# Performance work log

Hardware: AMD Instinct MI355X
Metric: run time of the kernel (lower is better)

The kernel has to match this reference:

```python
import jax, jax.numpy as jnp
import numpy as np

B, C, L, CH, CW = 2, 8, 512, 256, 8
NH = 8
FEATURES = 256
ROT = FEATURES // NH  # 32, partial rotary dim


def _rope(x, rot_dim):
    # x: (..., l, hd); rotate first rot_dim dims (interleaved pairs), pass rest through
    l = x.shape[-2]
    inv_freq = 1.0 / (10000.0 ** (jnp.arange(0, rot_dim, 2, dtype=jnp.float32) / rot_dim))
    freqs = jnp.arange(l, dtype=jnp.float32)[:, None] * inv_freq[None, :]  # (l, rot/2)
    freqs = jnp.repeat(freqs, 2, axis=-1)  # (l, rot)
    cos, sin = jnp.cos(freqs), jnp.sin(freqs)
    xr, xp = x[..., :rot_dim], x[..., rot_dim:]
    x2 = xr.reshape(xr.shape[:-1] + (rot_dim // 2, 2))
    rot = jnp.stack((-x2[..., 1], x2[..., 0]), axis=-1).reshape(xr.shape)
    return jnp.concatenate([xr * cos + rot * sin, xp], axis=-1)


def _conv(z, w):
    return jax.lax.conv_general_dilated(z, w, (1, 1), ((1, 1), (1, 1)),
                                        dimension_numbers=('NCHW', 'OIHW', 'NCHW'))


def _mlin(z, w):
    # per-channel linear over the height (features) axis: (n,c,h,w) x (c,g,h) -> (n,c,g,w)
    return jnp.einsum('nchw,cgh->ncgw', z, w)


def setup_inputs() -> dict:
    key = jax.random.key(0)
    ks = jax.random.split(key, 10)
    s_conv = 1.0 / np.sqrt(C * 9)
    s_lin = 1.0 / np.sqrt(FEATURES)
    return {
        'x': jax.random.normal(ks[0], (B, C, L, CH, CW), jnp.float32),
        'prev_qk': jax.random.normal(ks[1], (B, C, NH, L, L), jnp.float32),
        'conv_q_w': jax.random.normal(ks[2], (C, C, 3, 3), jnp.float32) * s_conv,
        'conv_k_w': jax.random.normal(ks[3], (C, C, 3, 3), jnp.float32) * s_conv,
        'conv_v_w': jax.random.normal(ks[4], (C, C, 3, 3), jnp.float32) * s_conv,
        'wq': jax.random.normal(ks[5], (C, FEATURES, FEATURES), jnp.float32) * s_lin,
        'wk': jax.random.normal(ks[6], (C, FEATURES, FEATURES), jnp.float32) * s_lin,
        'wv': jax.random.normal(ks[7], (C, FEATURES, FEATURES), jnp.float32) * s_lin,
        'wo': jax.random.normal(ks[8], (C, FEATURES, FEATURES), jnp.float32) * s_lin,
    }


def reference(x, prev_qk, conv_q_w, conv_k_w, conv_v_w, wq, wk, wv, wo):
    b, c, l, ch, cw = x.shape
    h = x.transpose(0, 2, 1, 3, 4).reshape(b * l, c, ch, cw)

    def heads(z):  # (b*l,c,ch,cw) -> (b,c,NH,l,hd)
        return (z.reshape(b, l, c, ch * cw).transpose(0, 2, 1, 3)
                 .reshape(b, c, l, NH, -1).transpose(0, 1, 3, 2, 4))

    q = heads(_mlin(_conv(h, conv_q_w), wq))
    k = heads(_mlin(_conv(h, conv_k_w), wk))
    v = heads(_mlin(_conv(h, conv_v_w), wv))

    q = _rope(q, ROT)
    k = _rope(k, ROT)

    qk = jnp.einsum('bcnld,bcnmd->bcnlm', q, k) / jnp.sqrt(jnp.float32(ch)) + prev_qk
    a = jnp.einsum('bcnlm,bcnmd->bcnld', jax.nn.softmax(qk, axis=-1), v)
    a = a.transpose(0, 1, 3, 2, 4).reshape(b, c, l, ch, cw)

    out = (_mlin(a.transpose(0, 2, 1, 3, 4).reshape(b * l, c, ch, cw), wo)
           .reshape(b, l, c, ch, cw).transpose(0, 2, 1, 3, 4))
    return out, qk
```

## Files before the change

kernel.cpp:

```cpp
#include <hip/hip_runtime.h>
#include <cstddef>
#include <cstdint>


typedef unsigned short u16;
typedef unsigned int u32;
typedef __attribute__((ext_vector_type(8))) short short8;
typedef __attribute__((ext_vector_type(4))) float floatx4;

__device__ __forceinline__ float bf2f(u16 u) {
  union { u32 i; float f; } v; v.i = ((u32)u) << 16; return v.f;
}
__device__ __forceinline__ u16 f2bf(float f) {
  union { float f; u32 i; } v; v.f = f;
  return (u16)((v.i + 0x7fffu + ((v.i >> 16) & 1u)) >> 16);
}

__global__ __launch_bounds__(256) void convert_w_kernel(
    const float* __restrict__ wq, const float* __restrict__ wk,
    const float* __restrict__ wv, const float* __restrict__ wo,
    u16* __restrict__ wbf) {
  int mat = blockIdx.y;
  const float* src = (mat == 0) ? wq : (mat == 1) ? wk : (mat == 2) ? wv : wo;
  int idx = blockIdx.x * 256 + threadIdx.x;
  wbf[(size_t)mat * 524288 + idx] = f2bf(src[idx]);
}

__global__ __launch_bounds__(256) void conv_fused_kernel(
    const float* __restrict__ x,
    const float* __restrict__ wq, const float* __restrict__ wk,
    const float* __restrict__ wv,
    u16* __restrict__ oq, u16* __restrict__ ok, u16* __restrict__ ov) {
  __shared__ float wl[1728];
  int t = threadIdx.x;
  for (int i2 = t; i2 < 1728; i2 += 256)
    wl[i2] = (i2 < 576) ? wq[i2] : (i2 < 1152 ? wk[i2 - 576] : wv[i2 - 1152]);
  __syncthreads();

  int bl = blockIdx.x >> 1, ih = blockIdx.x & 1;
  int b = bl >> 9, l = bl & 511;
  int il = t & 127, sh = t >> 7;
  int i = ih * 128 + il;

  float acc[12][8];
#pragma unroll
  for (int p = 0; p < 12; ++p)
#pragma unroll
    for (int j = 0; j < 8; ++j) acc[p][j] = 0.f;

  for (int ci = 0; ci < 8; ++ci) {
    const float* xc = x + (((size_t)(b * 8 + ci) * 512 + l) << 11);
    float xr[3][10];
#pragma unroll
    for (int di = 0; di < 3; ++di) {
      int gi = i + di - 1;
      xr[di][0] = 0.f; xr[di][9] = 0.f;
      if (gi >= 0 && gi < 256) {
        float4 a = *(const float4*)(xc + gi * 8);
        float4 bq = *(const float4*)(xc + gi * 8 + 4);
        xr[di][1] = a.x; xr[di][2] = a.y; xr[di][3] = a.z; xr[di][4] = a.w;
        xr[di][5] = bq.x; xr[di][6] = bq.y; xr[di][7] = bq.z; xr[di][8] = bq.w;
      } else {
#pragma unroll
        for (int j = 1; j < 9; ++j) xr[di][j] = 0.f;
      }
    }
#pragma unroll
    for (int p = 0; p < 12; ++p) {
      int pp = sh * 12 + p;
      int s = pp >> 3, co = pp & 7;
      const float* wp = &wl[s * 576 + (co * 8 + ci) * 9];
      float w00 = wp[0], w01 = wp[1], w02 = wp[2];
      float w10 = wp[3], w11 = wp[4], w12 = wp[5];
      float w20 = wp[6], w21 = wp[7], w22 = wp[8];
#pragma unroll
      for (int j = 0; j < 8; ++j) {
        acc[p][j] += w00 * xr[0][j] + w01 * xr[0][j + 1] + w02 * xr[0][j + 2]
                   + w10 * xr[1][j] + w11 * xr[1][j + 1] + w12 * xr[1][j + 2]
                   + w20 * xr[2][j] + w21 * xr[2][j + 1] + w22 * xr[2][j + 2];
      }
    }
  }
#pragma unroll
  for (int p = 0; p < 12; ++p) {
    int pp = sh * 12 + p;
    int s = pp >> 3, co = pp & 7;
    u16* ob = (s == 0) ? oq : (s == 1) ? ok : ov;
    size_t base = ((size_t)(bl * 8 + co)) << 11;
#pragma unroll
    for (int j = 0; j < 8; ++j) ob[base + j * 256 + i] = f2bf(acc[p][j]);
  }
}

template <int MODE>
__global__ __launch_bounds__(256) void mlin_mfma_kernel(
    const u16* __restrict__ zin,
    const u16* __restrict__ wbf,
    void* __restrict__ outp) {
  __shared__ u16 lds_a[8192];
  __shared__ u16 lds_b[8192];

  int tid = threadIdx.x;
  int wv = tid >> 6, lane = tid & 63;
  int fn = lane & 15, fq = lane >> 4;
  int wr = wv & 1, wc = wv >> 1;

  int bx = blockIdx.x;
  int c = bx >> 7;
  int cblk = (bx >> 1) & 63;
  int gblk = bx & 1;
  int g0 = gblk * 128;
  int col0 = cblk * 128;

  const u16* wsrc = wbf + ((size_t)c << 16);

  floatx4 acc[4][4];
#pragma unroll
  for (int mf = 0; mf < 4; ++mf)
#pragma unroll
    for (int nf = 0; nf < 4; ++nf) acc[mf][nf] = (floatx4){0.f, 0.f, 0.f, 0.f};

  for (int kt = 0; kt < 4; ++kt) {
    int h0 = kt * 64;
#pragma unroll
    for (int it = 0; it < 4; ++it) {
      int li = it * 256 + tid;
      int rr = li >> 3, hs = li & 7;
      uint4 ua = *(const uint4*)(wsrc + (size_t)(g0 + rr) * 256 + h0 + hs * 8);
      *(uint4*)((char*)lds_a + rr * 128 + ((hs ^ (rr & 7)) << 4)) = ua;
      uint4 ub = *(const uint4*)(zin +
          ((size_t)((cblk * 16 + (rr >> 3)) * 8 + c) << 11) + (rr & 7) * 256 +
          h0 + hs * 8);
      *(uint4*)((char*)lds_b + rr * 128 + ((hs ^ (rr & 7)) << 4)) = ub;
    }
    __syncthreads();
#pragma unroll
    for (int kc = 0; kc < 2; ++kc) {
      short8 af[4], bf[4];
#pragma unroll
      for (int mf = 0; mf < 4; ++mf) {
        int row = wr * 64 + mf * 16 + fn;
        af[mf] = *(const short8*)((const char*)lds_a + row * 128 +
                                  (((kc * 4 + fq) ^ (row & 7)) << 4));
      }
#pragma unroll
      for (int nf = 0; nf < 4; ++nf) {
        int row = wc * 64 + nf * 16 + fn;
        bf[nf] = *(const short8*)((const char*)lds_b + row * 128 +
                                  (((kc * 4 + fq) ^ (row & 7)) << 4));
      }
#pragma unroll
      for (int mf = 0; mf < 4; ++mf)
#pragma unroll
        for (int nf = 0; nf < 4; ++nf)
          acc[mf][nf] = __builtin_amdgcn_mfma_f32_16x16x32_bf16(
              af[mf], bf[nf], acc[mf][nf], 0, 0, 0);
    }
    __syncthreads();
  }

  if (MODE == 2) {
    float* op = (float*)outp;
#pragma unroll
    for (int nf = 0; nf < 4; ++nf) {
      int col = col0 + wc * 64 + nf * 16 + fn;
      int bl = col >> 3, w = col & 7;
      int b = bl >> 9, l = bl & 511;
      size_t rowoff = ((size_t)((b * 8 + c) * 512 + l) << 11) + w;
#pragma unroll
      for (int mf = 0; mf < 4; ++mf)
#pragma unroll
        for (int r = 0; r < 4; ++r) {
          int g = g0 + wr * 64 + mf * 16 + fq * 4 + r;
          op[rowoff + g * 8] = acc[mf][nf][r];
        }
    }
  } else {
    u16* op = (u16*)outp;
#pragma unroll
    for (int nf = 0; nf < 4; ++nf) {
      int col = col0 + wc * 64 + nf * 16 + fn;
      int bl = col >> 3, w = col & 7;
      int b = bl >> 9, l = bl & 511;
      size_t base = ((size_t)((b * 8 + c) * 8) << 17) + ((size_t)l << 8);
#pragma unroll
      for (int mf = 0; mf < 4; ++mf)
#pragma unroll
        for (int r = 0; r < 4; ++r) {
          int g = g0 + wr * 64 + mf * 16 + fq * 4 + r;
          float val = acc[mf][nf][r];
          if (MODE == 0) {
            float other = __shfl_xor(val, 1);
            int d = ((g & 31) << 3) + w;
            if (d < 32) {
              int p = d >> 1;
              float ang = (float)l * __expf(-(float)p * 0.57564627324851142f);
              float cv = cosf(ang), sv = sinf(ang);
              val = (d & 1) ? (val * cv + other * sv) : (val * cv - other * sv);
            }
          }
          int n = g >> 5, d2 = ((g & 31) << 3) + w;
          op[base + ((size_t)n << 17) + d2] = f2bf(val);
        }
    }
  }
}

__global__ __launch_bounds__(256) void transpose_v_kernel(const u16* __restrict__ vb,
                                                          u16* __restrict__ vt) {
  __shared__ u16 tile[64 * 66];
  int bx = blockIdx.x;
  int head = bx >> 5, mt = (bx >> 2) & 7, dt = bx & 3;
  size_t off = (size_t)head << 17;
  int t = threadIdx.x;
#pragma unroll
  for (int it = 0; it < 2; ++it) {
    int li = it * 256 + t;
    int r = li >> 3, cs = li & 7;
    uint4 u = *(const uint4*)(vb + off + (size_t)(mt * 64 + r) * 256 + dt * 64 + cs * 8);
    *(u32*)&tile[r * 66 + cs * 8 + 0] = u.x;
    *(u32*)&tile[r * 66 + cs * 8 + 2] = u.y;
    *(u32*)&tile[r * 66 + cs * 8 + 4] = u.z;
    *(u32*)&tile[r * 66 + cs * 8 + 6] = u.w;
  }
  __syncthreads();
#pragma unroll
  for (int it = 0; it < 2; ++it) {
    int li = it * 256 + t;
    int r = li >> 3, cs = li & 7;
    u16 tmp[8];
#pragma unroll
    for (int jj = 0; jj < 8; ++jj) tmp[jj] = tile[(cs * 8 + jj) * 66 + r];
    uint4 o;
    o.x = (u32)tmp[0] | ((u32)tmp[1] << 16);
    o.y = (u32)tmp[2] | ((u32)tmp[3] << 16);
    o.z = (u32)tmp[4] | ((u32)tmp[5] << 16);
    o.w = (u32)tmp[6] | ((u32)tmp[7] << 16);
    *(uint4*)(vt + off + (size_t)(dt * 64 + r) * 512 + mt * 64 + cs * 8) = o;
  }
}

__global__ __launch_bounds__(256, 4) void attn_kernel(
    const u16* __restrict__ q, const u16* __restrict__ k,
    const u16* __restrict__ vt, const float* __restrict__ prev,
    float* __restrict__ qk_out, u16* __restrict__ a2) {
  __shared__ u16 s_bf[32 * 520];
  __shared__ float rinv[32];

  int bx = blockIdx.x;
  int bid = (bx & 7) * 256 + (bx >> 3);
  int head = bid >> 4;
  int l0 = (bid & 15) << 5;
  int b = head >> 6, c = (head >> 3) & 7, nh = head & 7;
  size_t qoff = (size_t)head << 17;
  size_t poff = (size_t)head << 18;
  int tid = threadIdx.x;
  int w = tid >> 6, lane = tid & 63;
  int fn = lane & 15, fq = lane >> 4;
  int rt = w & 1, ct = w >> 1;

  short8 qf[8];
  const u16* qrow = q + qoff + (size_t)(l0 + rt * 16 + fn) * 256 + fq * 8;
#pragma unroll
  for (int kc = 0; kc < 8; ++kc) qf[kc] = *(const short8*)(qrow + kc * 32);

  const u16* kbase = k + qoff + (size_t)(ct * 16 + fn) * 256 + fq * 8;
  const float* prow = prev + poff + (size_t)(l0 + rt * 16 + fq * 4) * 512 + ct * 16 + fn;
  float* qrow_out = qk_out + poff + (size_t)(l0 + rt * 16 + fq * 4) * 512 + ct * 16 + fn;
#pragma unroll 2
  for (int mc = 0; mc < 16; ++mc) {
    int m0 = mc * 32;
    const u16* kr = kbase + ((size_t)m0 << 8);
    short8 bfr[8];
#pragma unroll
    for (int kc = 0; kc < 8; ++kc) bfr[kc] = *(const short8*)(kr + kc * 32);
    floatx4 acc = {0.f, 0.f, 0.f, 0.f};
#pragma unroll
    for (int kc = 0; kc < 8; ++kc)
      acc = __builtin_amdgcn_mfma_f32_16x16x32_bf16(qf[kc], bfr[kc], acc, 0, 0, 0);
    float pv[4];
#pragma unroll
    for (int r = 0; r < 4; ++r) pv[r] = prow[(size_t)r * 512 + m0];
#pragma unroll
    for (int r = 0; r < 4; ++r) {
      float sv = acc[r] * 0.0625f + pv[r];
      qrow_out[(size_t)r * 512 + m0] = sv;
      s_bf[(rt * 16 + fq * 4 + r) * 520 + m0 + ct * 16 + fn] = f2bf(sv);
    }
  }
  __syncthreads();

  {
    int srow = tid >> 3, sseg = tid & 7;
    u16* sp = &s_bf[srow * 520 + sseg * 8];
    float mx = -1e30f;
#pragma unroll
    for (int ii = 0; ii < 8; ++ii) {
      uint4 u = *(const uint4*)(sp + ii * 64);
      mx = fmaxf(mx, fmaxf(fmaxf(fmaxf(bf2f(u.x & 0xffff), bf2f(u.x >> 16)),
                                 fmaxf(bf2f(u.y & 0xffff), bf2f(u.y >> 16))),
                           fmaxf(fmaxf(bf2f(u.z & 0xffff), bf2f(u.z >> 16)),
                                 fmaxf(bf2f(u.w & 0xffff), bf2f(u.w >> 16)))));
    }
#pragma unroll
    for (int o = 1; o < 8; o <<= 1) mx = fmaxf(mx, __shfl_xor(mx, o));
    float sum = 0.f;
#pragma unroll
    for (int ii = 0; ii < 8; ++ii) {
      uint4 u = *(const uint4*)(sp + ii * 64);
      float e0 = __expf(bf2f(u.x & 0xffff) - mx), e1 = __expf(bf2f(u.x >> 16) - mx);
      float e2 = __expf(bf2f(u.y & 0xffff) - mx), e3 = __expf(bf2f(u.y >> 16) - mx);
      float e4 = __expf(bf2f(u.z & 0xffff) - mx), e5 = __expf(bf2f(u.z >> 16) - mx);
      float e6 = __expf(bf2f(u.w & 0xffff) - mx), e7 = __expf(bf2f(u.w >> 16) - mx);
      sum += e0 + e1 + e2 + e3 + e4 + e5 + e6 + e7;
      uint4 o;
      o.x = (u32)f2bf(e0) | ((u32)f2bf(e1) << 16);
      o.y = (u32)f2bf(e2) | ((u32)f2bf(e3) << 16);
      o.z = (u32)f2bf(e4) | ((u32)f2bf(e5) << 16);
      o.w = (u32)f2bf(e6) | ((u32)f2bf(e7) << 16);
      *(uint4*)(sp + ii * 64) = o;
    }
#pragma unroll
    for (int o = 1; o < 8; o <<= 1) sum += __shfl_xor(sum, o);
    if (sseg == 0) rinv[srow] = 1.0f / sum;
  }
  __syncthreads();

  floatx4 oacc[8];
#pragma unroll
  for (int dt = 0; dt < 8; ++dt) oacc[dt] = (floatx4){0.f, 0.f, 0.f, 0.f};

  const u16* vbase = vt + qoff + (size_t)(ct * 128 + fn) * 512 + fq * 8;
  const u16* arow = &s_bf[(rt * 16 + fn) * 520 + fq * 8];
#pragma unroll 2
  for (int mc = 0; mc < 16; ++mc) {
    int m0 = mc * 32;
    short8 af = *(const short8*)(arow + m0);
    short8 bfr[8];
#pragma unroll
    for (int dt = 0; dt < 8; ++dt)
      bfr[dt] = *(const short8*)(vbase + (size_t)dt * 16 * 512 + m0);
#pragma unroll
    for (int dt = 0; dt < 8; ++dt)
      oacc[dt] = __builtin_amdgcn_mfma_f32_16x16x32_bf16(af, bfr[dt], oacc[dt], 0, 0, 0);
  }

  float riv[4];
#pragma unroll
  for (int r = 0; r < 4; ++r) riv[r] = rinv[rt * 16 + fq * 4 + r];
#pragma unroll
  for (int dt = 0; dt < 8; ++dt) {
#pragma unroll
    for (int r = 0; r < 4; ++r) {
      int lrow = l0 + rt * 16 + fq * 4 + r;
      int d = ct * 128 + dt * 16 + fn;
      int bl = b * 512 + lrow;
      a2[(size_t)(bl * 8 + c) * 2048 + ((d & 7) << 8) + (nh << 5) + (d >> 3)] =
          f2bf(oacc[dt][r] * riv[r]);
    }
  }
}

extern "C" void kernel_launch(void* const* d_in, const int* in_sizes, int n_in,
                              void* d_out, int out_size, void* d_ws, size_t ws_size,
                              hipStream_t stream) {
  const float* x    = (const float*)d_in[0];
  const float* prev = (const float*)d_in[1];
  const float* cqw  = (const float*)d_in[2];
  const float* ckw  = (const float*)d_in[3];
  const float* cvw  = (const float*)d_in[4];
  const float* wq   = (const float*)d_in[5];
  const float* wk   = (const float*)d_in[6];
  const float* wv   = (const float*)d_in[7];
  const float* wo   = (const float*)d_in[8];

  float* out    = (float*)d_out;
  float* qk_out = out + 16777216;

  char* wsb = (char*)d_ws;
  u16* wbf    = (u16*)wsb;
  u16* convq  = (u16*)(wsb + 8388608);
  u16* convk  = convq + 16777216;
  u16* convv  = convk + 16777216;
  u16* qb     = convv + 16777216;
  u16* kb     = qb + 16777216;
  u16* vb     = kb + 16777216;
  u16* vtb    = vb + 16777216;
  u16* a2     = vtb + 16777216;

  convert_w_kernel<<<dim3(2048, 4), 256, 0, stream>>>(wq, wk, wv, wo, wbf);
  conv_fused_kernel<<<2048, 256, 0, stream>>>(x, cqw, ckw, cvw, convq, convk, convv);
  mlin_mfma_kernel<0><<<1024, 256, 0, stream>>>(convq, wbf, qb);
  mlin_mfma_kernel<0><<<1024, 256, 0, stream>>>(convk, wbf + 524288, kb);
  mlin_mfma_kernel<1><<<1024, 256, 0, stream>>>(convv, wbf + 1048576, vb);
  transpose_v_kernel<<<4096, 256, 0, stream>>>(vb, vtb);
  attn_kernel<<<2048, 256, 0, stream>>>(qb, kb, vtb, prev, qk_out, a2);
  mlin_mfma_kernel<2><<<1024, 256, 0, stream>>>(a2, wbf + 1572864, out);
}
```

Before: 812.9 us.

## Software-pipeline K/V and prev_qk loads in attention kernel with double buffering

Fully unrolls the QK and PV loops and double-buffers the K and V fragment loads, so the next chunk's global loads are issued before the current chunk's MFMAs. Prefetches prev_qk values eight chunks ahead into a register ring. Drops the min-blocks hint from launch bounds to allow more registers. The aim is to hide global memory latency behind matrix math, at the cost of higher register pressure and likely lower occupancy.

```diff
diff --git a/kernel.cpp b/kernel.cpp
--- a/kernel.cpp
+++ b/kernel.cpp
@@ -240,7 +240,7 @@
   }
 }
 
-__global__ __launch_bounds__(256, 4) void attn_kernel(
+__global__ __launch_bounds__(256) void attn_kernel(
     const u16* __restrict__ q, const u16* __restrict__ k,
     const u16* __restrict__ vt, const float* __restrict__ prev,
     float* __restrict__ qk_out, u16* __restrict__ a2) {
@@ -267,26 +267,44 @@
   const u16* kbase = k + qoff + (size_t)(ct * 16 + fn) * 256 + fq * 8;
   const float* prow = prev + poff + (size_t)(l0 + rt * 16 + fq * 4) * 512 + ct * 16 + fn;
   float* qrow_out = qk_out + poff + (size_t)(l0 + rt * 16 + fq * 4) * 512 + ct * 16 + fn;
-#pragma unroll 2
-  for (int mc = 0; mc < 16; ++mc) {
-    int m0 = mc * 32;
-    const u16* kr = kbase + ((size_t)m0 << 8);
-    short8 bfr[8];
-#pragma unroll
-    for (int kc = 0; kc < 8; ++kc) bfr[kc] = *(const short8*)(kr + kc * 32);
-    floatx4 acc = {0.f, 0.f, 0.f, 0.f};
-#pragma unroll
-    for (int kc = 0; kc < 8; ++kc)
-      acc = __builtin_amdgcn_mfma_f32_16x16x32_bf16(qf[kc], bfr[kc], acc, 0, 0, 0);
-    float pv[4];
-#pragma unroll
-    for (int r = 0; r < 4; ++r) pv[r] = prow[(size_t)r * 512 + m0];
-#pragma unroll
-    for (int r = 0; r < 4; ++r) {
-      float sv = acc[r] * 0.0625f + pv[r];
-      qrow_out[(size_t)r * 512 + m0] = sv;
-      s_bf[(rt * 16 + fq * 4 + r) * 520 + m0 + ct * 16 + fn] = f2bf(sv);
-    }
+
+  short8 kfa[8], kfb[8];
+  float pvb[8][4];
+
+#define LOADK(BUF, MC) do {                                                   \
+    const u16* _kr = kbase + ((size_t)((MC) * 32) << 8);                      \
+    _Pragma("unroll") for (int _kc = 0; _kc < 8; ++_kc)                       \
+      BUF[_kc] = *(const short8*)(_kr + _kc * 32);                            \
+  } while (0)
+
+#define LOADP(MC) do { if ((MC) < 16) {                                       \
+    _Pragma("unroll") for (int _r = 0; _r < 4; ++_r)                          \
+      pvb[(MC) & 7][_r] = prow[(size_t)_r * 512 + (MC) * 32];                 \
+  } } while (0)
+
+#define QKSTEP(BUF, MC) do {                                                  \
+    floatx4 _acc = {0.f, 0.f, 0.f, 0.f};                                      \
+    _Pragma("unroll") for (int _kc = 0; _kc < 8; ++_kc)                       \
+      _acc = __builtin_amdgcn_mfma_f32_16x16x32_bf16(qf[_kc], BUF[_kc], _acc, \
+                                                     0, 0, 0);                \
+    _Pragma("unroll") for (int _r = 0; _r < 4; ++_r) {                        \
+      float _sv = _acc[_r] * 0.0625f + pvb[(MC) & 7][_r];                     \
+      qrow_out[(size_t)_r * 512 + (MC) * 32] = _sv;                           \
+      s_bf[(rt * 16 + fq * 4 + _r) * 520 + (MC) * 32 + ct * 16 + fn] =        \
+          f2bf(_sv);                                                          \
+    }                                                                         \
+    LOADP((MC) + 8);                                                          \
+  } while (0)
+
+  LOADP(0); LOADP(1); LOADP(2); LOADP(3);
+  LOADP(4); LOADP(5); LOADP(6); LOADP(7);
+  LOADK(kfa, 0);
+#pragma unroll
+  for (int m2 = 0; m2 < 8; ++m2) {
+    LOADK(kfb, 2 * m2 + 1);
+    QKSTEP(kfa, 2 * m2);
+    if (m2 < 7) LOADK(kfa, 2 * m2 + 2);
+    QKSTEP(kfb, 2 * m2 + 1);
   }
   __syncthreads();
 
@@ -332,17 +350,29 @@
 
   const u16* vbase = vt + qoff + (size_t)(ct * 128 + fn) * 512 + fq * 8;
   const u16* arow = &s_bf[(rt * 16 + fn) * 520 + fq * 8];
-#pragma unroll 2
-  for (int mc = 0; mc < 16; ++mc) {
-    int m0 = mc * 32;
-    short8 af = *(const short8*)(arow + m0);
-    short8 bfr[8];
-#pragma unroll
-    for (int dt = 0; dt < 8; ++dt)
-      bfr[dt] = *(const short8*)(vbase + (size_t)dt * 16 * 512 + m0);
-#pragma unroll
-    for (int dt = 0; dt < 8; ++dt)
-      oacc[dt] = __builtin_amdgcn_mfma_f32_16x16x32_bf16(af, bfr[dt], oacc[dt], 0, 0, 0);
+
+  short8 vfa[8], vfb[8], afa, afb;
+
+#define LOADV(BUF, AF, MC) do {                                               \
+    const u16* _vr = vbase + (size_t)((MC) * 32);                             \
+    _Pragma("unroll") for (int _dt = 0; _dt < 8; ++_dt)                       \
+      BUF[_dt] = *(const short8*)(_vr + (size_t)_dt * 16 * 512);              \
+    AF = *(const short8*)(arow + (MC) * 32);                                  \
+  } while (0)
+
+#define PVSTEP(BUF, AF) do {                                                  \
+    _Pragma("unroll") for (int _dt = 0; _dt < 8; ++_dt)                       \
+      oacc[_dt] = __builtin_amdgcn_mfma_f32_16x16x32_bf16(AF, BUF[_dt],       \
+                                                          oacc[_dt], 0, 0, 0);\
+  } while (0)
+
+  LOADV(vfa, afa, 0);
+#pragma unroll
+  for (int m2 = 0; m2 < 8; ++m2) {
+    LOADV(vfb, afb, 2 * m2 + 1);
+    PVSTEP(vfa, afa);
+    if (m2 < 7) LOADV(vfa, afa, 2 * m2 + 2);
+    PVSTEP(vfb, afb);
   }
 
   float riv[4];
@@ -359,6 +389,11 @@
           f2bf(oacc[dt][r] * riv[r]);
     }
   }
+#undef LOADK
+#undef LOADP
+#undef QKSTEP
+#undef LOADV
+#undef PVSTEP
 }
 
 extern "C" void kernel_launch(void* const* d_in, const int* in_sizes, int n_in,
```

After: 814.9 us. Within noise of the previous version (+0.2%).

## Stage K and V tiles into swizzled LDS with async double buffering in attention

Applied to the files above, without the earlier changes.

The attention kernel now stages K and V tiles into shared memory with global_load_lds, double-buffered so the next tile loads while the current one feeds the MFMAs. The score and probability buffer and the staged tiles use XOR swizzles to avoid LDS bank conflicts, and the V transpose kernel writes a blocked layout to match. All prev_qk values are loaded up front into registers and qk is written after the loop. This raises register and LDS use and drops occupancy to 2 blocks per SM. It also adds a barrier on every iteration.

```diff
diff --git a/kernel.cpp b/kernel.cpp
--- a/kernel.cpp
+++ b/kernel.cpp
@@ -14,6 +14,11 @@
 __device__ __forceinline__ u16 f2bf(float f) {
   union { float f; u32 i; } v; v.f = f;
   return (u16)((v.i + 0x7fffu + ((v.i >> 16) & 1u)) >> 16);
+}
+__device__ __forceinline__ void gl_lds16(const void* g, void* l) {
+  __builtin_amdgcn_global_load_lds(
+      (__attribute__((address_space(1))) void*)(g),
+      (__attribute__((address_space(3))) void*)(l), 16, 0, 0);
 }
 
 __global__ __launch_bounds__(256) void convert_w_kernel(
@@ -236,16 +241,20 @@
     o.y = (u32)tmp[2] | ((u32)tmp[3] << 16);
     o.z = (u32)tmp[4] | ((u32)tmp[5] << 16);
     o.w = (u32)tmp[6] | ((u32)tmp[7] << 16);
-    *(uint4*)(vt + off + (size_t)(dt * 64 + r) * 512 + mt * 64 + cs * 8) = o;
-  }
-}
-
-__global__ __launch_bounds__(256, 4) void attn_kernel(
+    int d = dt * 64 + r;
+    *(uint4*)(vt + off + (size_t)(mt * 2 + (cs >> 2)) * 8192 + (size_t)d * 32 +
+              (cs & 3) * 8) = o;
+  }
+}
+
+__global__ __launch_bounds__(256, 2) void attn_kernel(
     const u16* __restrict__ q, const u16* __restrict__ k,
     const u16* __restrict__ vt, const float* __restrict__ prev,
     float* __restrict__ qk_out, u16* __restrict__ a2) {
-  __shared__ u16 s_bf[32 * 520];
-  __shared__ float rinv[32];
+  __shared__ uint4 sbuf4[2048];
+  __shared__ uint4 pbuf4[2048];
+  char* stage = (char*)sbuf4;
+  char* sbb = (char*)pbuf4;
 
   int bx = blockIdx.x;
   int bid = (bx & 7) * 256 + (bx >> 3);
@@ -258,45 +267,75 @@
   int w = tid >> 6, lane = tid & 63;
   int fn = lane & 15, fq = lane >> 4;
   int rt = w & 1, ct = w >> 1;
+  int krow = ct * 16 + fn;
+
+#define STAGE_K(CUR, M0) do {                                                 \
+    _Pragma("unroll") for (int _it = 0; _it < 4; ++_it) {                     \
+      int _rr = (w << 3) + (_it << 1) + (lane >> 5);                          \
+      const u16* _g = k + qoff + ((size_t)((M0) + _rr) << 8) +                \
+                      (((lane & 31) ^ (_rr & 7)) << 3);                       \
+      gl_lds16(_g, stage + (CUR) * 16384 + (((w << 3) + (_it << 1)) << 9));   \
+    } } while (0)
+
+#define STAGE_V(CUR, MC) do {                                                 \
+    _Pragma("unroll") for (int _it = 0; _it < 4; ++_it) {                     \
+      int _d = (w << 6) + (_it << 4) + (lane >> 2);                           \
+      const u16* _g = vt + qoff + ((size_t)(MC) << 13) + (_d << 5) +          \
+                      (((lane & 3) ^ ((_d >> 1) & 3)) << 3);                  \
+      gl_lds16(_g, stage + (CUR) * 16384 + (((w << 6) + (_it << 4)) << 6));   \
+    } } while (0)
 
   short8 qf[8];
   const u16* qrow = q + qoff + (size_t)(l0 + rt * 16 + fn) * 256 + fq * 8;
 #pragma unroll
   for (int kc = 0; kc < 8; ++kc) qf[kc] = *(const short8*)(qrow + kc * 32);
 
-  const u16* kbase = k + qoff + (size_t)(ct * 16 + fn) * 256 + fq * 8;
+  float pv[16][4];
   const float* prow = prev + poff + (size_t)(l0 + rt * 16 + fq * 4) * 512 + ct * 16 + fn;
+#pragma unroll
+  for (int mc = 0; mc < 16; ++mc)
+#pragma unroll
+    for (int r = 0; r < 4; ++r) pv[mc][r] = prow[r * 512 + mc * 32];
+
+  STAGE_K(0, 0);
+  __syncthreads();
+
+#pragma unroll
+  for (int mc = 0; mc < 16; ++mc) {
+    if (mc < 15) STAGE_K((mc + 1) & 1, (mc + 1) * 32);
+    floatx4 acc = {0.f, 0.f, 0.f, 0.f};
+#pragma unroll
+    for (int kc = 0; kc < 8; ++kc) {
+      short8 bfr = *(const short8*)(stage + ((mc & 1) << 14) + (krow << 9) +
+                                    ((((kc << 2) + fq) ^ (fn & 7)) << 4));
+      acc = __builtin_amdgcn_mfma_f32_16x16x32_bf16(qf[kc], bfr, acc, 0, 0, 0);
+    }
+#pragma unroll
+    for (int r = 0; r < 4; ++r) {
+      float sv = acc[r] * 0.0625f + pv[mc][r];
+      pv[mc][r] = sv;
+      int row = rt * 16 + fq * 4 + r;
+      *(u16*)(sbb + (row << 10) +
+              ((((mc << 2) + (ct << 1) + (fn >> 3)) ^ (row & 7)) << 4) +
+              ((fn & 7) << 1)) = f2bf(sv);
+    }
+    __syncthreads();
+  }
+
   float* qrow_out = qk_out + poff + (size_t)(l0 + rt * 16 + fq * 4) * 512 + ct * 16 + fn;
-#pragma unroll 2
-  for (int mc = 0; mc < 16; ++mc) {
-    int m0 = mc * 32;
-    const u16* kr = kbase + ((size_t)m0 << 8);
-    short8 bfr[8];
-#pragma unroll
-    for (int kc = 0; kc < 8; ++kc) bfr[kc] = *(const short8*)(kr + kc * 32);
-    floatx4 acc = {0.f, 0.f, 0.f, 0.f};
-#pragma unroll
-    for (int kc = 0; kc < 8; ++kc)
-      acc = __builtin_amdgcn_mfma_f32_16x16x32_bf16(qf[kc], bfr[kc], acc, 0, 0, 0);
-    float pv[4];
-#pragma unroll
-    for (int r = 0; r < 4; ++r) pv[r] = prow[(size_t)r * 512 + m0];
-#pragma unroll
-    for (int r = 0; r < 4; ++r) {
-      float sv = acc[r] * 0.0625f + pv[r];
-      qrow_out[(size_t)r * 512 + m0] = sv;
-      s_bf[(rt * 16 + fq * 4 + r) * 520 + m0 + ct * 16 + fn] = f2bf(sv);
-    }
-  }
-  __syncthreads();
+#pragma unroll
+  for (int mc = 0; mc < 16; ++mc)
+#pragma unroll
+    for (int r = 0; r < 4; ++r) qrow_out[r * 512 + mc * 32] = pv[mc][r];
 
   {
     int srow = tid >> 3, sseg = tid & 7;
-    u16* sp = &s_bf[srow * 520 + sseg * 8];
+    int ss = sseg ^ (srow & 7);
+    char* sp = sbb + (srow << 10);
     float mx = -1e30f;
 #pragma unroll
     for (int ii = 0; ii < 8; ++ii) {
-      uint4 u = *(const uint4*)(sp + ii * 64);
+      uint4 u = *(const uint4*)(sp + (((ii << 3) + ss) << 4));
       mx = fmaxf(mx, fmaxf(fmaxf(fmaxf(bf2f(u.x & 0xffff), bf2f(u.x >> 16)),
                                  fmaxf(bf2f(u.y & 0xffff), bf2f(u.y >> 16))),
                            fmaxf(fmaxf(bf2f(u.z & 0xffff), bf2f(u.z >> 16)),
@@ -307,7 +346,7 @@
     float sum = 0.f;
 #pragma unroll
     for (int ii = 0; ii < 8; ++ii) {
-      uint4 u = *(const uint4*)(sp + ii * 64);
+      uint4 u = *(const uint4*)(sp + (((ii << 3) + ss) << 4));
       float e0 = __expf(bf2f(u.x & 0xffff) - mx), e1 = __expf(bf2f(u.x >> 16) - mx);
       float e2 = __expf(bf2f(u.y & 0xffff) - mx), e3 = __expf(bf2f(u.y >> 16) - mx);
       float e4 = __expf(bf2f(u.z & 0xffff) - mx), e5 = __expf(bf2f(u.z >> 16) - mx);
@@ -318,36 +357,42 @@
       o.y = (u32)f2bf(e2) | ((u32)f2bf(e3) << 16);
       o.z = (u32)f2bf(e4) | ((u32)f2bf(e5) << 16);
       o.w = (u32)f2bf(e6) | ((u32)f2bf(e7) << 16);
-      *(uint4*)(sp + ii * 64) = o;
+      *(uint4*)(sp + (((ii << 3) + ss) << 4)) = o;
     }
 #pragma unroll
     for (int o = 1; o < 8; o <<= 1) sum += __shfl_xor(sum, o);
-    if (sseg == 0) rinv[srow] = 1.0f / sum;
+    if (sseg == 0) ((float*)(stage + 16384))[srow] = 1.0f / sum;
   }
   __syncthreads();
 
+  float riv[4];
+#pragma unroll
+  for (int r = 0; r < 4; ++r)
+    riv[r] = ((const float*)(stage + 16384))[rt * 16 + fq * 4 + r];
+  STAGE_V(0, 0);
+  __syncthreads();
+
   floatx4 oacc[8];
 #pragma unroll
   for (int dt = 0; dt < 8; ++dt) oacc[dt] = (floatx4){0.f, 0.f, 0.f, 0.f};
 
-  const u16* vbase = vt + qoff + (size_t)(ct * 128 + fn) * 512 + fq * 8;
-  const u16* arow = &s_bf[(rt * 16 + fn) * 520 + fq * 8];
-#pragma unroll 2
+  int prowp = rt * 16 + fn;
+  int vswz = (fn >> 1) & 3;
+#pragma unroll
   for (int mc = 0; mc < 16; ++mc) {
-    int m0 = mc * 32;
-    short8 af = *(const short8*)(arow + m0);
-    short8 bfr[8];
-#pragma unroll
-    for (int dt = 0; dt < 8; ++dt)
-      bfr[dt] = *(const short8*)(vbase + (size_t)dt * 16 * 512 + m0);
-#pragma unroll
-    for (int dt = 0; dt < 8; ++dt)
-      oacc[dt] = __builtin_amdgcn_mfma_f32_16x16x32_bf16(af, bfr[dt], oacc[dt], 0, 0, 0);
-  }
-
-  float riv[4];
-#pragma unroll
-  for (int r = 0; r < 4; ++r) riv[r] = rinv[rt * 16 + fq * 4 + r];
+    if (mc < 15) STAGE_V((mc + 1) & 1, mc + 1);
+    short8 af = *(const short8*)(sbb + (prowp << 10) +
+                                 ((((mc << 2) + fq) ^ (fn & 7)) << 4));
+#pragma unroll
+    for (int dt = 0; dt < 8; ++dt) {
+      int d = ct * 128 + dt * 16 + fn;
+      short8 bv = *(const short8*)(stage + ((mc & 1) << 14) + (d << 6) +
+                                   ((fq ^ vswz) << 4));
+      oacc[dt] = __builtin_amdgcn_mfma_f32_16x16x32_bf16(af, bv, oacc[dt], 0, 0, 0);
+    }
+    if (mc < 15) __syncthreads();
+  }
+
 #pragma unroll
   for (int dt = 0; dt < 8; ++dt) {
 #pragma unroll
@@ -359,6 +404,8 @@
           f2bf(oacc[dt][r] * riv[r]);
     }
   }
+#undef STAGE_K
+#undef STAGE_V
 }
 
 extern "C" void kernel_launch(void* const* d_in, const int* in_sizes, int n_in,
```

New measurement: 716.4 us. -11.9%, faster.
